# Kernel tuning notes

Measured on AMD Instinct MI355X. Metric: run time of the kernel, lower is better.

The kernel has to match this reference:

```python
import jax, jax.numpy as jnp
import numpy as np

DIM = 256
HEADS = 8
B, T, D, H, W = 2, 8, 16, 16, 16


def _mha(x, wqkv, bqkv, wo, bo):
    # x: [M, S, F]; standard self-attention (q=k=v=x), LoRA rank 0.
    M, S, F = x.shape
    hd = F // HEADS
    qkv = jnp.einsum('msf,kfg->kmsg', x, wqkv) + bqkv[:, None, None, :]  # [3,M,S,F]
    q, k, v = qkv
    q = q.reshape(M, S, HEADS, hd).transpose(0, 2, 1, 3)  # [M,Hh,S,hd]
    k = k.reshape(M, S, HEADS, hd).transpose(0, 2, 1, 3)
    v = v.reshape(M, S, HEADS, hd).transpose(0, 2, 1, 3)
    scores = jnp.einsum('mhsd,mhtd->mhst', q, k) / jnp.sqrt(jnp.asarray(hd, x.dtype))
    attn = jax.nn.softmax(scores, axis=-1)
    out = jnp.einsum('mhst,mhtd->mhsd', attn, v)
    out = out.transpose(0, 2, 1, 3).reshape(M, S, F)
    return out @ wo + bo


def _make_params(key, name_suffix):
    k1, k2 = jax.random.split(key)
    s = 1.0 / np.sqrt(DIM)
    return {
        f'wqkv_{name_suffix}': jax.random.normal(k1, (3, DIM, DIM), jnp.float32) * s,
        f'bqkv_{name_suffix}': jnp.zeros((3, DIM), jnp.float32),
        f'wo_{name_suffix}': jax.random.normal(k2, (DIM, DIM), jnp.float32) * s,
        f'bo_{name_suffix}': jnp.zeros((DIM,), jnp.float32),
    }


def setup_inputs() -> dict:
    key = jax.random.key(0)
    ks = jax.random.split(key, 5)
    inp = {'x': jax.random.normal(ks[0], (B, T, D * H * W, DIM), jnp.float32)}
    for k, ax in zip(ks[1:], ['t', 'd', 'h', 'w']):
        inp.update(_make_params(k, ax))
    inp['grid_d'] = D
    inp['grid_h'] = H
    inp['grid_w'] = W
    return inp


def reference(x, wqkv_t, bqkv_t, wo_t, bo_t,
              wqkv_d, bqkv_d, wo_d, bo_d,
              wqkv_h, bqkv_h, wo_h, bo_h,
              wqkv_w, bqkv_w, wo_w, bo_w,
              grid_d, grid_h, grid_w):
    b, t, n, f = x.shape
    d, h, w = grid_d, grid_h, grid_w
    x = x.reshape(b, t, d, h, w, f)
    if t > 1:
        xt = x.transpose(0, 2, 3, 4, 1, 5).reshape(b * d * h * w, t, f)
        xt = _mha(xt, wqkv_t, bqkv_t, wo_t, bo_t)
        xt = xt.reshape(b, d, h, w, t, f).transpose(0, 4, 1, 2, 3, 5)
        x = x + xt
    xd = x.transpose(0, 1, 3, 4, 2, 5).reshape(b * t * h * w, d, f)
    xd = _mha(xd, wqkv_d, bqkv_d, wo_d, bo_d)
    xd = xd.reshape(b, t, h, w, d, f).transpose(0, 1, 4, 2, 3, 5)
    xh = x.transpose(0, 1, 2, 4, 3, 5).reshape(b * t * d * w, h, f)
    xh = _mha(xh, wqkv_h, bqkv_h, wo_h, bo_h)
    xh = xh.reshape(b, t, d, w, h, f).transpose(0, 1, 2, 4, 3, 5)
    xw = x.reshape(b * t * d * h, w, f)
    xw = _mha(xw, wqkv_w, bqkv_w, wo_w, bo_w)
    xw = xw.reshape(b, t, d, h, w, f)
    x_comb = x + xd + xh + xw
    return x_comb.reshape(b, t, d * h * w, f)
```

## Files before the change

kernel.cpp:

```cpp
#include <hip/hip_runtime.h>

typedef __attribute__((ext_vector_type(4))) float f32x4;
typedef __attribute__((ext_vector_type(8))) short s16x8;

__device__ __forceinline__ ushort f2bf(float f) {
  union { float f; uint u; } v; v.f = f;
  uint r = v.u + 0x7fffu + ((v.u >> 16) & 1u);
  return (ushort)(r >> 16);
}

__device__ __forceinline__ void glds16(const void* g, void* l) {
  __builtin_amdgcn_global_load_lds(
      (const __attribute__((address_space(1))) uint*)g,
      (__attribute__((address_space(3))) uint*)l, 16, 0, 0);
}

__device__ __forceinline__ int asidx(int row, int col) {
  return row*256 + ((((col>>3) ^ (row & 7)))<<3) + (col&7);
}
__device__ __forceinline__ int scridx(int row, int col) {
  return row*32 + ((((col>>3) ^ ((row>>2)&3)))<<3) + (col&7);
}
__device__ __forceinline__ int epidx(int row, int f) {
  return row*256 + (f ^ ((row & 7) << 2));
}

struct WSrc { const float* p[8]; };

__global__ __launch_bounds__(256) void prep_weights(WSrc s, ushort* wq, ushort* wo) {
  int mm = blockIdx.x >> 6;
  int t  = blockIdx.x & 63;
  int a = mm >> 2, sub = mm & 3;
  const float* src = (sub < 3) ? (s.p[a*2] + sub*65536) : s.p[a*2+1];
  ushort*      dst = (sub < 3) ? (wq + (a*3 + sub)*65536) : (wo + a*65536);
  int gt = (t >> 3) * 32, ft = (t & 7) * 32;
  __shared__ float tile[32][33];
  int lx = threadIdx.x & 31, ly = threadIdx.x >> 5;
#pragma unroll
  for (int i = 0; i < 4; i++)
    tile[ly + i*8][lx] = src[(ft + ly + i*8)*256 + gt + lx];
  __syncthreads();
#pragma unroll
  for (int i = 0; i < 4; i++) {
    int n = gt + ly + i*8, col = ft + lx;
    dst[asidx(n, col)] = f2bf(tile[lx][ly + i*8]);
  }
}

template<int AXIS>
__device__ __forceinline__ int token_index(int blk, int row) {
  if (AXIS == 0) {
    int seq = blk*8 + (row >> 3);
    int t = row & 7;
    int b = seq >> 12, n = seq & 4095;
    return (b*8 + t)*4096 + n;
  } else {
    int sid = blk*4 + (row >> 4);
    int bt = sid >> 8, lo = sid & 255, r = row & 15;
    if (AXIS == 1) { int hh = lo >> 4, ww = lo & 15; return bt*4096 + r*256 + hh*16 + ww; }
    if (AXIS == 2) { int dd = lo >> 4, ww = lo & 15; return bt*4096 + dd*256 + r*16 + ww; }
    { int dd = lo >> 4, hh = lo & 15; return bt*4096 + dd*256 + hh*16 + r; }
  }
}

#define PUB_BARRIER() do { \
    __builtin_amdgcn_sched_barrier(0); \
    asm volatile("s_waitcnt lgkmcnt(0)" ::: "memory"); \
    __builtin_amdgcn_sched_barrier(0); \
    __builtin_amdgcn_s_barrier(); \
    __builtin_amdgcn_sched_barrier(0); } while (0)

template<int AXIS>
__global__ __launch_bounds__(256, 2) void axial_pass(
    const float* __restrict__ x0, const ushort* __restrict__ xb,
    const ushort* __restrict__ wqkvT, const float* __restrict__ bqkv,
    const ushort* __restrict__ woT, const float* __restrict__ bo,
    float* __restrict__ out, ushort* __restrict__ x1b) {

  __shared__ ushort smem[40960];
  ushort* Wb0 = smem;
  ushort* Wb1 = smem + 8192;
  ushort* AsT = smem + 16384;
  ushort* Scr = smem + 32768;

  const int tid = threadIdx.x, blk = blockIdx.x;
  const int wv = tid >> 6, lane = tid & 63, llo = lane & 15, lhi = lane >> 4;
  const int rg = wv >> 1, ch = wv & 1;
  const f32x4 fzero = {0.f, 0.f, 0.f, 0.f};
  const s16x8 szero = {0,0,0,0,0,0,0,0};

  auto issue_stage = [&](int s) {
    const ushort* src = (s < 24) ? (wqkvT + (s % 3)*65536 + (s / 3)*8192)
                                 : (woT + (s - 24)*8192);
    const ushort* g = src + wv*2048 + lane*8;
    ushort* l = ((s & 1) ? Wb1 : Wb0) + wv*2048;
#pragma unroll
    for (int i = 0; i < 4; i++) glds16(g + i*512, l + i*512);
  };

#define STAGE_SYNC(sn) do { \
    __builtin_amdgcn_sched_barrier(0); \
    asm volatile("s_waitcnt vmcnt(0) lgkmcnt(0)" ::: "memory"); \
    __builtin_amdgcn_sched_barrier(0); \
    __builtin_amdgcn_s_barrier(); \
    __builtin_amdgcn_sched_barrier(0); \
    if ((sn) < 32) issue_stage(sn); \
  } while (0)

  issue_stage(0);

  {
    int row = tid >> 2, q = tid & 3;
    int tok = token_index<AXIS>(blk, row);
    if (AXIS == 0) {
      const float4* s4 = (const float4*)(x0 + (size_t)tok*256 + q*64);
#pragma unroll
      for (int c2 = 0; c2 < 8; c2++) {
        float4 v0 = s4[c2*2], v1 = s4[c2*2 + 1];
        s16x8 o;
        o[0] = (short)f2bf(v0.x); o[1] = (short)f2bf(v0.y);
        o[2] = (short)f2bf(v0.z); o[3] = (short)f2bf(v0.w);
        o[4] = (short)f2bf(v1.x); o[5] = (short)f2bf(v1.y);
        o[6] = (short)f2bf(v1.z); o[7] = (short)f2bf(v1.w);
        *(s16x8*)(AsT + asidx(row, (q*8 + c2)*8)) = o;
      }
    } else {
      const s16x8* s8 = (const s16x8*)(xb + (size_t)tok*256 + q*64);
#pragma unroll
      for (int c2 = 0; c2 < 8; c2++)
        *(s16x8*)(AsT + asidx(row, (q*8 + c2)*8)) = s8[c2];
    }
  }
  {
    ushort* Vtw = Scr + wv*2048 + 1024;
    *(s16x8*)(Vtw + scridx(lane >> 1, 16 + (lane & 1)*8)) = szero;
  }
  __syncthreads();

  s16x8 af[2][8];
#pragma unroll
  for (int g = 0; g < 2; g++)
#pragma unroll
    for (int ks = 0; ks < 8; ks++)
      af[g][ks] = *(const s16x8*)(AsT + asidx(rg*32 + g*16 + llo, (ks*4 + lhi)*8));

  auto proj2 = [&](int sb, f32x4& c0, f32x4& c1) {
    const ushort* buf = sb ? Wb1 : Wb0;
    __builtin_amdgcn_s_setprio(1);
#pragma unroll
    for (int ks = 0; ks < 8; ks++) {
      s16x8 bv = *(const s16x8*)(buf + asidx(ch*16 + llo, (ks*4 + lhi)*8));
      c0 = __builtin_amdgcn_mfma_f32_16x16x32_bf16(af[0][ks], bv, c0, 0, 0, 0);
      c1 = __builtin_amdgcn_mfma_f32_16x16x32_bf16(af[1][ks], bv, c1, 0, 0, 0);
    }
    __builtin_amdgcn_s_setprio(0);
  };

#pragma unroll 1
  for (int h = 0; h < 8; h++) {
    STAGE_SYNC(3*h + 1);
    {
      f32x4 c0 = fzero, c1 = fzero;
      proj2((3*h) & 1, c0, c1);
      float bi = bqkv[h*32 + ch*16 + llo];
      ushort* q0 = Scr + (rg*2 + 0)*2048;
      ushort* q1 = Scr + (rg*2 + 1)*2048;
#pragma unroll
      for (int r = 0; r < 4; r++) {
        q0[scridx(lhi*4 + r, ch*16 + llo)] = f2bf(c0[r] + bi);
        q1[scridx(lhi*4 + r, ch*16 + llo)] = f2bf(c1[r] + bi);
      }
    }
    STAGE_SYNC(3*h + 2);
    {
      f32x4 c0 = fzero, c1 = fzero;
      proj2((3*h + 1) & 1, c0, c1);
      float bi = bqkv[256 + h*32 + ch*16 + llo];
      ushort* k0 = Scr + (rg*2 + 0)*2048 + 512;
      ushort* k1 = Scr + (rg*2 + 1)*2048 + 512;
#pragma unroll
      for (int r = 0; r < 4; r++) {
        k0[scridx(lhi*4 + r, ch*16 + llo)] = f2bf(c0[r] + bi);
        k1[scridx(lhi*4 + r, ch*16 + llo)] = f2bf(c1[r] + bi);
      }
    }
    STAGE_SYNC(3*h + 3);
    {
      f32x4 c0 = fzero, c1 = fzero;
      proj2((3*h + 2) & 1, c0, c1);
      float bi = bqkv[512 + h*32 + ch*16 + llo];
      ushort* v0 = Scr + (rg*2 + 0)*2048 + 1024;
      ushort* v1 = Scr + (rg*2 + 1)*2048 + 1024;
#pragma unroll
      for (int r = 0; r < 4; r++) {
        v0[scridx(ch*16 + llo, lhi*4 + r)] = f2bf(c0[r] + bi);
        v1[scridx(ch*16 + llo, lhi*4 + r)] = f2bf(c1[r] + bi);
      }
    }
    PUB_BARRIER();

    {
      ushort* S = Scr + wv*2048;
      s16x8 aq = *(const s16x8*)(S + scridx(llo, lhi*8));
      s16x8 bk = *(const s16x8*)(S + 512 + scridx(llo, lhi*8));
      f32x4 sc = __builtin_amdgcn_mfma_f32_16x16x32_bf16(aq, bk, fzero, 0, 0, 0);
#pragma unroll
      for (int r = 0; r < 4; r++) {
        float sv = sc[r] * 0.17677669529663689f;
        if (AXIS == 0) {
          int srow = lhi*4 + r;
          if ((srow >> 3) != (llo >> 3)) sv = -1e30f;
        }
        float mx = sv;
        mx = fmaxf(mx, __shfl_xor(mx, 1));
        mx = fmaxf(mx, __shfl_xor(mx, 2));
        mx = fmaxf(mx, __shfl_xor(mx, 4));
        mx = fmaxf(mx, __shfl_xor(mx, 8));
        float e = __expf(sv - mx);
        float sm = e;
        sm += __shfl_xor(sm, 1);
        sm += __shfl_xor(sm, 2);
        sm += __shfl_xor(sm, 4);
        sm += __shfl_xor(sm, 8);
        (S + 512)[scridx(lhi*4 + r, llo)] = f2bf(e * __builtin_amdgcn_rcpf(sm));
      }
      s16x8 ap  = *(const s16x8*)(S + 512 + scridx(llo, lhi*8));
      s16x8 bv0 = *(const s16x8*)(S + 1024 + scridx(llo, lhi*8));
      s16x8 bv1 = *(const s16x8*)(S + 1024 + scridx(16 + llo, lhi*8));
      f32x4 o0 = __builtin_amdgcn_mfma_f32_16x16x32_bf16(ap, bv0, fzero, 0, 0, 0);
      f32x4 o1 = __builtin_amdgcn_mfma_f32_16x16x32_bf16(ap, bv1, fzero, 0, 0, 0);
#pragma unroll
      for (int r = 0; r < 4; r++) {
        AsT[asidx(wv*16 + lhi*4 + r, h*32 + llo)]      = f2bf(o0[r]);
        AsT[asidx(wv*16 + lhi*4 + r, h*32 + 16 + llo)] = f2bf(o1[r]);
      }
    }
  }

  PUB_BARRIER();

#pragma unroll
  for (int g = 0; g < 2; g++)
#pragma unroll
    for (int ks = 0; ks < 8; ks++)
      af[g][ks] = *(const s16x8*)(AsT + asidx(rg*32 + g*16 + llo, (ks*4 + lhi)*8));

  f32x4 acc[16];
#pragma unroll
  for (int i = 0; i < 16; i++) acc[i] = fzero;
#pragma unroll
  for (int st = 0; st < 8; st++) {
    STAGE_SYNC(25 + st);
    const ushort* buf = (st & 1) ? Wb1 : Wb0;
    __builtin_amdgcn_s_setprio(1);
#pragma unroll
    for (int ks = 0; ks < 8; ks++) {
      s16x8 bv = *(const s16x8*)(buf + asidx(ch*16 + llo, (ks*4 + lhi)*8));
      acc[st*2]   = __builtin_amdgcn_mfma_f32_16x16x32_bf16(af[0][ks], bv, acc[st*2],   0, 0, 0);
      acc[st*2+1] = __builtin_amdgcn_mfma_f32_16x16x32_bf16(af[1][ks], bv, acc[st*2+1], 0, 0, 0);
    }
    __builtin_amdgcn_s_setprio(0);
  }

  float* Fep = (float*)smem;
  PUB_BARRIER();
#pragma unroll
  for (int st = 0; st < 8; st++) {
#pragma unroll
    for (int g = 0; g < 2; g++) {
#pragma unroll
      for (int r = 0; r < 4; r++) {
        int row = rg*32 + g*16 + lhi*4 + r;
        Fep[epidx(row, st*32 + ch*16 + llo)] = acc[st*2 + g][r];
      }
    }
  }
  PUB_BARRIER();
  {
    int rbase = tid >> 3, g = tid & 7;
#pragma unroll 1
    for (int step = 0; step < 2; step++) {
      int row = rbase + step*32;
      int tok = token_index<AXIS>(blk, row);
      size_t base = (size_t)tok*256;
#pragma unroll
      for (int i = 0; i < 8; i++) {
        int f = i*32 + g*4;
        float4 v = *(float4*)&Fep[epidx(row, f)];
        float4 b = *(const float4*)&bo[f];
        v.x += b.x; v.y += b.y; v.z += b.z; v.w += b.w;
        if (AXIS == 0) {
          float4 x = *(const float4*)&x0[base + f];
          v.x += x.x; v.y += x.y; v.z += x.z; v.w += x.w;
          *(float4*)&out[base + f] = v;
          ushort4 p; p.x = f2bf(v.x); p.y = f2bf(v.y);
          p.z = f2bf(v.z); p.w = f2bf(v.w);
          *(ushort4*)&x1b[base + f] = p;
        } else {
          float4 o = *(float4*)&out[base + f];
          o.x += v.x; o.y += v.y; o.z += v.z; o.w += v.w;
          *(float4*)&out[base + f] = o;
        }
      }
    }
  }
#undef STAGE_SYNC
}

extern "C" void kernel_launch(void* const* d_in, const int* in_sizes, int n_in,
                              void* d_out, int out_size, void* d_ws, size_t ws_size,
                              hipStream_t stream) {
  const float* x = (const float*)d_in[0];
  ushort* wq  = (ushort*)d_ws;
  ushort* wo  = wq + 4*3*65536;
  ushort* x1b = wo + 4*65536;
  float* out = (float*)d_out;

  WSrc wsrc;
  wsrc.p[0] = (const float*)d_in[1];  wsrc.p[1] = (const float*)d_in[3];
  wsrc.p[2] = (const float*)d_in[5];  wsrc.p[3] = (const float*)d_in[7];
  wsrc.p[4] = (const float*)d_in[9];  wsrc.p[5] = (const float*)d_in[11];
  wsrc.p[6] = (const float*)d_in[13]; wsrc.p[7] = (const float*)d_in[15];
  prep_weights<<<dim3(1024), dim3(256), 0, stream>>>(wsrc, wq, wo);

  const float* bq_t = (const float*)d_in[2];  const float* bo_t = (const float*)d_in[4];
  const float* bq_d = (const float*)d_in[6];  const float* bo_d = (const float*)d_in[8];
  const float* bq_h = (const float*)d_in[10]; const float* bo_h = (const float*)d_in[12];
  const float* bq_w = (const float*)d_in[14]; const float* bo_w = (const float*)d_in[16];

  axial_pass<0><<<dim3(1024), dim3(256), 0, stream>>>(x, nullptr, wq + 0*3*65536, bq_t, wo + 0*65536, bo_t, out, x1b);
  axial_pass<1><<<dim3(1024), dim3(256), 0, stream>>>(nullptr, x1b, wq + 1*3*65536, bq_d, wo + 1*65536, bo_d, out, nullptr);
  axial_pass<2><<<dim3(1024), dim3(256), 0, stream>>>(nullptr, x1b, wq + 2*3*65536, bq_h, wo + 2*65536, bo_h, out, nullptr);
  axial_pass<3><<<dim3(1024), dim3(256), 0, stream>>>(nullptr, x1b, wq + 3*3*65536, bq_w, wo + 3*65536, bo_w, out, nullptr);
}
```

Before: 351.0 us.

## Triple-buffer weight stages with prefetch depth two and keep attention output in registers

Weight staging moves from two LDS buffers with a full vmcnt(0) wait per stage to three rotating buffers. Stage s+2 is issued while stage s is consumed, and the wait is relaxed to vmcnt(4). Each wave now keeps its attention output for every head in registers (af_o), so the separate AsT output buffer and its reload before the output projection are gone. The output projection is remapped so each wave owns 16 rows and all 32 columns per stage. LDS use drops from 80KB to 64KB and global-load latency hiding improves, at the cost of more registers and a fully unrolled head loop.

```diff
diff --git a/kernel.cpp b/kernel.cpp
--- a/kernel.cpp
+++ b/kernel.cpp
@@ -77,11 +77,8 @@
     const ushort* __restrict__ woT, const float* __restrict__ bo,
     float* __restrict__ out, ushort* __restrict__ x1b) {
 
-  __shared__ ushort smem[40960];
-  ushort* Wb0 = smem;
-  ushort* Wb1 = smem + 8192;
-  ushort* AsT = smem + 16384;
-  ushort* Scr = smem + 32768;
+  __shared__ ushort smem[32768];
+  ushort* Scr = smem + 24576;
 
   const int tid = threadIdx.x, blk = blockIdx.x;
   const int wv = tid >> 6, lane = tid & 63, llo = lane & 15, lhi = lane >> 4;
@@ -93,21 +90,20 @@
     const ushort* src = (s < 24) ? (wqkvT + (s % 3)*65536 + (s / 3)*8192)
                                  : (woT + (s - 24)*8192);
     const ushort* g = src + wv*2048 + lane*8;
-    ushort* l = ((s & 1) ? Wb1 : Wb0) + wv*2048;
+    ushort* l = smem + (s % 3)*8192 + wv*2048;
 #pragma unroll
     for (int i = 0; i < 4; i++) glds16(g + i*512, l + i*512);
   };
 
-#define STAGE_SYNC(sn) do { \
-    __builtin_amdgcn_sched_barrier(0); \
-    asm volatile("s_waitcnt vmcnt(0) lgkmcnt(0)" ::: "memory"); \
+#define STAGE_SYNC(s) do { \
+    __builtin_amdgcn_sched_barrier(0); \
+    if ((s) < 31) { asm volatile("s_waitcnt vmcnt(4) lgkmcnt(0)" ::: "memory"); } \
+    else          { asm volatile("s_waitcnt vmcnt(0) lgkmcnt(0)" ::: "memory"); } \
     __builtin_amdgcn_sched_barrier(0); \
     __builtin_amdgcn_s_barrier(); \
     __builtin_amdgcn_sched_barrier(0); \
-    if ((sn) < 32) issue_stage(sn); \
+    if ((s) + 2 < 32) issue_stage((s) + 2); \
   } while (0)
-
-  issue_stage(0);
 
   {
     int row = tid >> 2, q = tid & 3;
@@ -122,13 +118,13 @@
         o[2] = (short)f2bf(v0.z); o[3] = (short)f2bf(v0.w);
         o[4] = (short)f2bf(v1.x); o[5] = (short)f2bf(v1.y);
         o[6] = (short)f2bf(v1.z); o[7] = (short)f2bf(v1.w);
-        *(s16x8*)(AsT + asidx(row, (q*8 + c2)*8)) = o;
+        *(s16x8*)(smem + asidx(row, (q*8 + c2)*8)) = o;
       }
     } else {
       const s16x8* s8 = (const s16x8*)(xb + (size_t)tok*256 + q*64);
 #pragma unroll
       for (int c2 = 0; c2 < 8; c2++)
-        *(s16x8*)(AsT + asidx(row, (q*8 + c2)*8)) = s8[c2];
+        *(s16x8*)(smem + asidx(row, (q*8 + c2)*8)) = s8[c2];
     }
   }
   {
@@ -142,10 +138,13 @@
   for (int g = 0; g < 2; g++)
 #pragma unroll
     for (int ks = 0; ks < 8; ks++)
-      af[g][ks] = *(const s16x8*)(AsT + asidx(rg*32 + g*16 + llo, (ks*4 + lhi)*8));
-
-  auto proj2 = [&](int sb, f32x4& c0, f32x4& c1) {
-    const ushort* buf = sb ? Wb1 : Wb0;
+      af[g][ks] = *(const s16x8*)(smem + asidx(rg*32 + g*16 + llo, (ks*4 + lhi)*8));
+  __syncthreads();
+
+  issue_stage(0);
+  issue_stage(1);
+
+  auto proj2 = [&](const ushort* buf, f32x4& c0, f32x4& c1) {
     __builtin_amdgcn_s_setprio(1);
 #pragma unroll
     for (int ks = 0; ks < 8; ks++) {
@@ -156,38 +155,40 @@
     __builtin_amdgcn_s_setprio(0);
   };
 
-#pragma unroll 1
+  s16x8 af_o[8];
+
+#pragma unroll
   for (int h = 0; h < 8; h++) {
+    STAGE_SYNC(3*h);
+    {
+      f32x4 c0 = fzero, c1 = fzero;
+      proj2(smem + ((3*h) % 3)*8192, c0, c1);
+      float bi = bqkv[h*32 + ch*16 + llo];
+      ushort* q0 = Scr + (rg*2 + 0)*2048;
+      ushort* q1 = Scr + (rg*2 + 1)*2048;
+#pragma unroll
+      for (int r = 0; r < 4; r++) {
+        q0[scridx(lhi*4 + r, ch*16 + llo)] = f2bf(c0[r] + bi);
+        q1[scridx(lhi*4 + r, ch*16 + llo)] = f2bf(c1[r] + bi);
+      }
+    }
     STAGE_SYNC(3*h + 1);
     {
       f32x4 c0 = fzero, c1 = fzero;
-      proj2((3*h) & 1, c0, c1);
-      float bi = bqkv[h*32 + ch*16 + llo];
-      ushort* q0 = Scr + (rg*2 + 0)*2048;
-      ushort* q1 = Scr + (rg*2 + 1)*2048;
-#pragma unroll
-      for (int r = 0; r < 4; r++) {
-        q0[scridx(lhi*4 + r, ch*16 + llo)] = f2bf(c0[r] + bi);
-        q1[scridx(lhi*4 + r, ch*16 + llo)] = f2bf(c1[r] + bi);
+      proj2(smem + ((3*h + 1) % 3)*8192, c0, c1);
+      float bi = bqkv[256 + h*32 + ch*16 + llo];
+      ushort* k0 = Scr + (rg*2 + 0)*2048 + 512;
+      ushort* k1 = Scr + (rg*2 + 1)*2048 + 512;
+#pragma unroll
+      for (int r = 0; r < 4; r++) {
+        k0[scridx(lhi*4 + r, ch*16 + llo)] = f2bf(c0[r] + bi);
+        k1[scridx(lhi*4 + r, ch*16 + llo)] = f2bf(c1[r] + bi);
       }
     }
     STAGE_SYNC(3*h + 2);
     {
       f32x4 c0 = fzero, c1 = fzero;
-      proj2((3*h + 1) & 1, c0, c1);
-      float bi = bqkv[256 + h*32 + ch*16 + llo];
-      ushort* k0 = Scr + (rg*2 + 0)*2048 + 512;
-      ushort* k1 = Scr + (rg*2 + 1)*2048 + 512;
-#pragma unroll
-      for (int r = 0; r < 4; r++) {
-        k0[scridx(lhi*4 + r, ch*16 + llo)] = f2bf(c0[r] + bi);
-        k1[scridx(lhi*4 + r, ch*16 + llo)] = f2bf(c1[r] + bi);
-      }
-    }
-    STAGE_SYNC(3*h + 3);
-    {
-      f32x4 c0 = fzero, c1 = fzero;
-      proj2((3*h + 2) & 1, c0, c1);
+      proj2(smem + ((3*h + 2) % 3)*8192, c0, c1);
       float bi = bqkv[512 + h*32 + ch*16 + llo];
       ushort* v0 = Scr + (rg*2 + 0)*2048 + 1024;
       ushort* v1 = Scr + (rg*2 + 1)*2048 + 1024;
@@ -196,10 +197,8 @@
         v0[scridx(ch*16 + llo, lhi*4 + r)] = f2bf(c0[r] + bi);
         v1[scridx(ch*16 + llo, lhi*4 + r)] = f2bf(c1[r] + bi);
       }
-    }
-    PUB_BARRIER();
-
-    {
+      PUB_BARRIER();
+
       ushort* S = Scr + wv*2048;
       s16x8 aq = *(const s16x8*)(S + scridx(llo, lhi*8));
       s16x8 bk = *(const s16x8*)(S + 512 + scridx(llo, lhi*8));
@@ -231,33 +230,27 @@
       f32x4 o1 = __builtin_amdgcn_mfma_f32_16x16x32_bf16(ap, bv1, fzero, 0, 0, 0);
 #pragma unroll
       for (int r = 0; r < 4; r++) {
-        AsT[asidx(wv*16 + lhi*4 + r, h*32 + llo)]      = f2bf(o0[r]);
-        AsT[asidx(wv*16 + lhi*4 + r, h*32 + 16 + llo)] = f2bf(o1[r]);
-      }
-    }
-  }
-
-  PUB_BARRIER();
-
-#pragma unroll
-  for (int g = 0; g < 2; g++)
-#pragma unroll
-    for (int ks = 0; ks < 8; ks++)
-      af[g][ks] = *(const s16x8*)(AsT + asidx(rg*32 + g*16 + llo, (ks*4 + lhi)*8));
+        S[scridx(lhi*4 + r, llo)]      = f2bf(o0[r]);
+        S[scridx(lhi*4 + r, 16 + llo)] = f2bf(o1[r]);
+      }
+      af_o[h] = *(const s16x8*)(S + scridx(llo, lhi*8));
+    }
+  }
 
   f32x4 acc[16];
 #pragma unroll
   for (int i = 0; i < 16; i++) acc[i] = fzero;
 #pragma unroll
   for (int st = 0; st < 8; st++) {
-    STAGE_SYNC(25 + st);
-    const ushort* buf = (st & 1) ? Wb1 : Wb0;
+    STAGE_SYNC(24 + st);
+    const ushort* buf = smem + ((24 + st) % 3)*8192;
     __builtin_amdgcn_s_setprio(1);
 #pragma unroll
     for (int ks = 0; ks < 8; ks++) {
-      s16x8 bv = *(const s16x8*)(buf + asidx(ch*16 + llo, (ks*4 + lhi)*8));
-      acc[st*2]   = __builtin_amdgcn_mfma_f32_16x16x32_bf16(af[0][ks], bv, acc[st*2],   0, 0, 0);
-      acc[st*2+1] = __builtin_amdgcn_mfma_f32_16x16x32_bf16(af[1][ks], bv, acc[st*2+1], 0, 0, 0);
+      s16x8 b0 = *(const s16x8*)(buf + asidx(llo,      (ks*4 + lhi)*8));
+      s16x8 b1 = *(const s16x8*)(buf + asidx(16 + llo, (ks*4 + lhi)*8));
+      acc[st*2]   = __builtin_amdgcn_mfma_f32_16x16x32_bf16(af_o[ks], b0, acc[st*2],   0, 0, 0);
+      acc[st*2+1] = __builtin_amdgcn_mfma_f32_16x16x32_bf16(af_o[ks], b1, acc[st*2+1], 0, 0, 0);
     }
     __builtin_amdgcn_s_setprio(0);
   }
@@ -267,11 +260,11 @@
 #pragma unroll
   for (int st = 0; st < 8; st++) {
 #pragma unroll
-    for (int g = 0; g < 2; g++) {
-#pragma unroll
-      for (int r = 0; r < 4; r++) {
-        int row = rg*32 + g*16 + lhi*4 + r;
-        Fep[epidx(row, st*32 + ch*16 + llo)] = acc[st*2 + g][r];
+    for (int j = 0; j < 2; j++) {
+#pragma unroll
+      for (int r = 0; r < 4; r++) {
+        int row = wv*16 + lhi*4 + r;
+        Fep[epidx(row, st*32 + j*16 + llo)] = acc[st*2 + j][r];
       }
     }
   }
```

Measured after the change: 350.3 us (median of 3 runs). No clear change (-0.2%).
